# Optimization experiments

Hardware: AMD Instinct MI355X
Metric: run time of the kernel (lower is better)

Reference implementation:

```python
import jax, jax.numpy as jnp
import numpy as np
from jax import lax

B, T, D_IN, D_OUT = 8, 4096, 256, 256


def setup_inputs() -> dict:
    key = jax.random.key(0)
    k1, k2, k3, k4, k5 = jax.random.split(key, 5)
    bound_in = 1.0 / np.sqrt(D_IN)
    return {
        "inputs": jax.random.normal(k1, (B, T, D_IN), dtype=jnp.float32),
        "mask": jnp.zeros((B, T, 1), dtype=jnp.float32),
        "W_in": jax.random.uniform(k2, (D_OUT, D_IN), jnp.float32, -bound_in, bound_in),
        "b_in": jax.random.uniform(k3, (D_OUT,), jnp.float32, -bound_in, bound_in),
        "W_f": jax.random.uniform(k4, (D_OUT, D_IN), jnp.float32, -bound_in, bound_in),
        "b_f": jax.random.uniform(k5, (D_OUT,), jnp.float32, -bound_in, bound_in),
    }


def _forget_mult(f, x):
    # h_t = f_t * x_t + (1 - f_t) * h_{t-1}, h_{-1} = 0 (torchqrnn ForgetMult, hidden_init=None)
    fT = jnp.swapaxes(f, 0, 1)  # (T, B, D)
    xT = jnp.swapaxes(x, 0, 1)

    def step(h, fx):
        ft, xt = fx
        h = ft * xt + (1.0 - ft) * h
        return h, h

    h0 = jnp.zeros(xT.shape[1:], dtype=x.dtype)  # (B, D)
    _, hs = lax.scan(step, h0, (fT, xT))
    return jnp.swapaxes(hs, 0, 1)  # (B, T, D)


def reference(inputs, mask, W_in, b_in, W_f, b_f):
    # right_to_left = False -> no flips
    x = jnp.tanh(jnp.einsum("btd,od->bto", inputs, W_in) + b_in)
    f = jax.nn.sigmoid(jnp.einsum("btd,od->bto", inputs, W_f) + b_f + mask * 10000.0)
    return _forget_mult(f, x)
```

## Files before the change

kernel.cpp:

```cpp
#include <hip/hip_runtime.h>
#include <math.h>


typedef _Float16 f16x8 __attribute__((ext_vector_type(8)));
typedef float f32x4 __attribute__((ext_vector_type(4)));
typedef float f32x16 __attribute__((ext_vector_type(16)));
typedef unsigned int u32x4 __attribute__((ext_vector_type(4)));

constexpr int B_ = 8, T_ = 4096, D_ = 256, K_ = 256;
constexpr int M_ = B_ * T_;
constexpr int CHUNK = 64;
constexpr int NCH = T_ / CHUNK;
constexpr int NBLK = M_ / CHUNK;
constexpr int SLICE_EL = 8192;

struct alignas(4) XF { _Float16 x, f; };
struct alignas(4) HP2 { _Float16 h, p; };
union UHP { unsigned int u; HP2 hp; XF xf; };

__device__ __forceinline__ float fexp2(float a) { return __builtin_amdgcn_exp2f(a); }
__device__ __forceinline__ float frcp(float a) { return __builtin_amdgcn_rcpf(a); }
constexpr float L2E = 1.4426950408889634f;

__device__ __forceinline__ float fast_sigmoid(float z) {
  return frcp(1.f + fexp2(-z * L2E));
}
__device__ __forceinline__ float fast_tanh(float z) {
  const float t = fexp2(-2.f * L2E * fabsf(z));
  return copysignf((1.f - t) * frcp(1.f + t), z);
}

__global__ __launch_bounds__(256) void wconv(const float* __restrict__ Win,
                                             const float* __restrict__ Wf,
                                             _Float16* __restrict__ Wh2) {
  const int t = blockIdx.x * 256 + threadIdx.x;
  const int n = t & 255;
  const int kc = (t >> 8) & 1;
  const int mat = (t >> 9) & 1;
  const int kk2 = t >> 10;
  const float* s = (mat ? Wf : Win) + (size_t)n * K_ + kk2 * 16 + kc * 8;
  f32x4 a = *(const f32x4*)s;
  f32x4 b = *(const f32x4*)(s + 4);
  f16x8 o;
  o[0] = (_Float16)a[0]; o[1] = (_Float16)a[1];
  o[2] = (_Float16)a[2]; o[3] = (_Float16)a[3];
  o[4] = (_Float16)b[0]; o[5] = (_Float16)b[1];
  o[6] = (_Float16)b[2]; o[7] = (_Float16)b[3];
  *(f16x8*)(Wh2 + (size_t)t * 8) = o;
}

__global__ __launch_bounds__(256, 3) void gemm_hp(
    const float* __restrict__ A, const _Float16* __restrict__ Wh2,
    const float* __restrict__ bin, const float* __restrict__ bfv,
    const float* __restrict__ mask, unsigned int* __restrict__ HPout,
    float* __restrict__ Ap, float* __restrict__ Hp) {
  __shared__ __align__(16) char smem[49152];
  char* ldsA = smem;
  char* ldsW = smem + 32768;

  const int tid = threadIdx.x;
  const int w = tid >> 6, lane = tid & 63;
  const int mw = w >> 1, nw = w & 1;
  const int nl = lane & 31, kh = lane >> 5;
  const int ml = mw * 32 + nl;
  const int g = blockIdx.x;
  const int row0 = g * CHUNK;

  f32x16 acc[2][4];
#pragma unroll
  for (int mat = 0; mat < 2; ++mat)
#pragma unroll
    for (int nt = 0; nt < 4; ++nt) acc[mat][nt] = (f32x16)(0.f);

  {
    const int am = tid >> 2;
    const int ak4 = (tid & 3) * 8;
    const float* agp = A + (size_t)(row0 + am) * K_ + ak4 * 8;
#pragma unroll
    for (int j = 0; j < 8; ++j) {
      const int kcg = ak4 + j;
      f32x4 lo = *(const f32x4*)(agp + j * 8);
      f32x4 hi = *(const f32x4*)(agp + j * 8 + 4);
      f16x8 t;
      t[0] = (_Float16)lo[0]; t[1] = (_Float16)lo[1];
      t[2] = (_Float16)lo[2]; t[3] = (_Float16)lo[3];
      t[4] = (_Float16)hi[0]; t[5] = (_Float16)hi[1];
      t[6] = (_Float16)hi[2]; t[7] = (_Float16)hi[3];
      *(f16x8*)(ldsA + am * 512 + ((kcg ^ (am & 31)) << 4)) = t;
    }
  }
  __syncthreads();

  f16x8 wreg[4];
#pragma unroll
  for (int j = 0; j < 4; ++j)
    wreg[j] = *(const f16x8*)(Wh2 + (size_t)(j * 256 + tid) * 8);

  for (int kk2 = 0; kk2 < 16; ++kk2) {
#pragma unroll
    for (int j = 0; j < 4; ++j)
      *(f16x8*)(ldsW + (size_t)(j * 256 + tid) * 16) = wreg[j];
    if (kk2 < 15) {
#pragma unroll
      for (int j = 0; j < 4; ++j)
        wreg[j] = *(const f16x8*)(Wh2 + (size_t)(kk2 + 1) * SLICE_EL +
                                  (size_t)(j * 256 + tid) * 8);
    }
    __syncthreads();
    f16x8 afr;
    {
      const int kcg = kk2 * 2 + kh;
      afr = *(const f16x8*)(ldsA + ml * 512 + ((kcg ^ (ml & 31)) << 4));
    }
#pragma unroll
    for (int mat = 0; mat < 2; ++mat)
#pragma unroll
      for (int nt = 0; nt < 4; ++nt) {
        const int n = nw * 128 + nt * 32 + nl;
        f16x8 bfr = *(const f16x8*)(ldsW + (size_t)((mat * 2 + kh) * 256 + n) * 16);
        acc[mat][nt] = __builtin_amdgcn_mfma_f32_32x32x16_f16(
            afr, bfr, acc[mat][nt], 0, 0, 0);
      }
    __syncthreads();
  }

  float bx[4], bf[4];
#pragma unroll
  for (int nt = 0; nt < 4; ++nt) {
    const int col = nw * 128 + nt * 32 + nl;
    bx[nt] = bin[col];
    bf[nt] = bfv[col];
  }
  float madd[16];
#pragma unroll
  for (int reg = 0; reg < 16; ++reg) {
    const int rl = mw * 32 + (reg & 3) + 8 * (reg >> 2) + 4 * kh;
    madd[reg] = 10000.f * mask[row0 + rl];
  }

  const int d = tid;
  float hrun = 0.f, Prun = 1.f;
#pragma unroll
  for (int p = 0; p < 2; ++p) {
    if (mw == p) {
#pragma unroll
      for (int nt = 0; nt < 4; ++nt) {
        const int col = nw * 128 + nt * 32 + nl;
#pragma unroll
        for (int reg = 0; reg < 16; ++reg) {
          const int rloc = (reg & 3) + 8 * (reg >> 2) + 4 * kh;
          const float zx = acc[0][nt][reg] + bx[nt];
          const float zf = acc[1][nt][reg] + bf[nt] + madd[reg];
          XF v;
          v.x = (_Float16)fast_tanh(zx);
          v.f = (_Float16)fast_sigmoid(zf);
          *(XF*)(smem + ((size_t)rloc * D_ + col) * 4) = v;
        }
      }
    }
    __syncthreads();
#pragma unroll 8
    for (int t = 0; t < 32; ++t) {
      char* slot = smem + ((size_t)t * D_ + d) * 4;
      const XF v = *(const XF*)slot;
      const float f = (float)v.f;
      const float a = 1.f - f;
      hrun = f * (float)v.x + a * hrun;
      Prun *= a;
      HP2 o;
      o.h = (_Float16)hrun;
      o.p = (_Float16)Prun;
      *(HP2*)slot = o;
    }
    __syncthreads();
#pragma unroll
    for (int j = 0; j < 8; ++j) {
      const int c = j * 256 + tid;
      u32x4 vv = *(const u32x4*)(smem + (size_t)c * 16);
      *(u32x4*)(HPout + (size_t)g * 16384 + (size_t)p * 8192 + (size_t)c * 4) = vv;
    }
    __syncthreads();
  }

  Ap[(size_t)g * D_ + d] = Prun;
  Hp[(size_t)g * D_ + d] = hrun;
}

__global__ __launch_bounds__(256) void scan_mid(const float* __restrict__ Ap,
                                                const float* __restrict__ Hp,
                                                float* __restrict__ hs) {
  const int b = blockIdx.x, d = threadIdx.x;
  float h = 0.f;
#pragma unroll 8
  for (int c = 0; c < NCH; ++c) {
    const size_t i = ((size_t)(b * NCH + c)) * D_ + d;
    hs[i] = h;
    h = Hp[i] + Ap[i] * h;
  }
}

__global__ __launch_bounds__(256) void final_k(const unsigned int* __restrict__ HP,
                                               const float* __restrict__ hs,
                                               float* __restrict__ out) {
  const int g = blockIdx.x;
  const int lane = threadIdx.x & 63, wv = threadIdx.x >> 6;
  const int d0 = lane * 4;
  const f32x4 h0 = *(const f32x4*)(hs + (size_t)g * D_ + d0);
#pragma unroll 4
  for (int tt = 0; tt < 16; ++tt) {
    const int t = wv * 16 + tt;
    const size_t idx = ((size_t)g * CHUNK + t) * D_ + d0;
    u32x4 u = *(const u32x4*)(HP + idx);
    f32x4 o;
#pragma unroll
    for (int i = 0; i < 4; ++i) {
      UHP q; q.u = u[i];
      o[i] = (float)q.hp.h + (float)q.hp.p * h0[i];
    }
    *(f32x4*)(out + idx) = o;
  }
}

extern "C" void kernel_launch(void* const* d_in, const int* in_sizes, int n_in,
                              void* d_out, int out_size, void* d_ws, size_t ws_size,
                              hipStream_t stream) {
  const float* inputs = (const float*)d_in[0];
  const float* mask   = (const float*)d_in[1];
  const float* W_in   = (const float*)d_in[2];
  const float* b_in   = (const float*)d_in[3];
  const float* W_f    = (const float*)d_in[4];
  const float* b_f    = (const float*)d_in[5];
  float* out = (float*)d_out;
  char* ws = (char*)d_ws;

  constexpr size_t HPSZ = (size_t)M_ * D_ * 4;
  constexpr size_t WSZ  = (size_t)2 * 256 * 256 * 2;
  constexpr size_t SUM  = (size_t)NBLK * D_ * sizeof(float);

  unsigned int* HPb = (unsigned int*)ws;
  _Float16* Wh2 = (_Float16*)(ws + HPSZ);
  float* Ap = (float*)(ws + HPSZ + WSZ);
  float* Hp = (float*)(ws + HPSZ + WSZ + SUM);
  float* hs = (float*)(ws + HPSZ + WSZ + 2 * SUM);

  wconv<<<64, 256, 0, stream>>>(W_in, W_f, Wh2);
  gemm_hp<<<NBLK, 256, 0, stream>>>(inputs, Wh2, b_in, b_f, mask, HPb, Ap, Hp);
  scan_mid<<<B_, 256, 0, stream>>>(Ap, Hp, hs);
  final_k<<<NBLK, 256, 0, stream>>>(HPb, hs, out);
}
```

Measured before the change: 128.0 us.

## Fold cross-chunk scan into final kernel and retile GEMM waves over columns

```diff
diff --git a/kernel.cpp b/kernel.cpp
--- a/kernel.cpp
+++ b/kernel.cpp
@@ -60,17 +60,17 @@
 
   const int tid = threadIdx.x;
   const int w = tid >> 6, lane = tid & 63;
-  const int mw = w >> 1, nw = w & 1;
   const int nl = lane & 31, kh = lane >> 5;
-  const int ml = mw * 32 + nl;
   const int g = blockIdx.x;
   const int row0 = g * CHUNK;
 
-  f32x16 acc[2][4];
+  f32x16 acc[2][2][2];
 #pragma unroll
   for (int mat = 0; mat < 2; ++mat)
 #pragma unroll
-    for (int nt = 0; nt < 4; ++nt) acc[mat][nt] = (f32x16)(0.f);
+    for (int mt = 0; mt < 2; ++mt)
+#pragma unroll
+      for (int nt = 0; nt < 2; ++nt) acc[mat][mt][nt] = (f32x16)(0.f);
 
   {
     const int am = tid >> 2;
@@ -107,55 +107,59 @@
                                   (size_t)(j * 256 + tid) * 8);
     }
     __syncthreads();
-    f16x8 afr;
-    {
+    f16x8 afr[2];
+#pragma unroll
+    for (int mt = 0; mt < 2; ++mt) {
+      const int ml = mt * 32 + nl;
       const int kcg = kk2 * 2 + kh;
-      afr = *(const f16x8*)(ldsA + ml * 512 + ((kcg ^ (ml & 31)) << 4));
+      afr[mt] = *(const f16x8*)(ldsA + ml * 512 + ((kcg ^ (ml & 31)) << 4));
     }
 #pragma unroll
     for (int mat = 0; mat < 2; ++mat)
 #pragma unroll
-      for (int nt = 0; nt < 4; ++nt) {
-        const int n = nw * 128 + nt * 32 + nl;
+      for (int nt = 0; nt < 2; ++nt) {
+        const int n = w * 64 + nt * 32 + nl;
         f16x8 bfr = *(const f16x8*)(ldsW + (size_t)((mat * 2 + kh) * 256 + n) * 16);
-        acc[mat][nt] = __builtin_amdgcn_mfma_f32_32x32x16_f16(
-            afr, bfr, acc[mat][nt], 0, 0, 0);
+#pragma unroll
+        for (int mt = 0; mt < 2; ++mt)
+          acc[mat][mt][nt] = __builtin_amdgcn_mfma_f32_32x32x16_f16(
+              afr[mt], bfr, acc[mat][mt][nt], 0, 0, 0);
       }
     __syncthreads();
   }
 
-  float bx[4], bf[4];
-#pragma unroll
-  for (int nt = 0; nt < 4; ++nt) {
-    const int col = nw * 128 + nt * 32 + nl;
+  float bx[2], bf[2];
+#pragma unroll
+  for (int nt = 0; nt < 2; ++nt) {
+    const int col = w * 64 + nt * 32 + nl;
     bx[nt] = bin[col];
     bf[nt] = bfv[col];
   }
-  float madd[16];
-#pragma unroll
-  for (int reg = 0; reg < 16; ++reg) {
-    const int rl = mw * 32 + (reg & 3) + 8 * (reg >> 2) + 4 * kh;
-    madd[reg] = 10000.f * mask[row0 + rl];
-  }
+  float madd[2][16];
+#pragma unroll
+  for (int mt = 0; mt < 2; ++mt)
+#pragma unroll
+    for (int reg = 0; reg < 16; ++reg) {
+      const int rl = mt * 32 + (reg & 3) + 8 * (reg >> 2) + 4 * kh;
+      madd[mt][reg] = 10000.f * mask[row0 + rl];
+    }
 
   const int d = tid;
   float hrun = 0.f, Prun = 1.f;
 #pragma unroll
   for (int p = 0; p < 2; ++p) {
-    if (mw == p) {
-#pragma unroll
-      for (int nt = 0; nt < 4; ++nt) {
-        const int col = nw * 128 + nt * 32 + nl;
-#pragma unroll
-        for (int reg = 0; reg < 16; ++reg) {
-          const int rloc = (reg & 3) + 8 * (reg >> 2) + 4 * kh;
-          const float zx = acc[0][nt][reg] + bx[nt];
-          const float zf = acc[1][nt][reg] + bf[nt] + madd[reg];
-          XF v;
-          v.x = (_Float16)fast_tanh(zx);
-          v.f = (_Float16)fast_sigmoid(zf);
-          *(XF*)(smem + ((size_t)rloc * D_ + col) * 4) = v;
-        }
+#pragma unroll
+    for (int nt = 0; nt < 2; ++nt) {
+      const int col = w * 64 + nt * 32 + nl;
+#pragma unroll
+      for (int reg = 0; reg < 16; ++reg) {
+        const int rloc = (reg & 3) + 8 * (reg >> 2) + 4 * kh;
+        const float zx = acc[0][p][nt][reg] + bx[nt];
+        const float zf = acc[1][p][nt][reg] + bf[nt] + madd[p][reg];
+        XF v;
+        v.x = (_Float16)fast_tanh(zx);
+        v.f = (_Float16)fast_sigmoid(zf);
+        *(XF*)(smem + ((size_t)rloc * D_ + col) * 4) = v;
       }
     }
     __syncthreads();
@@ -186,26 +190,25 @@
   Hp[(size_t)g * D_ + d] = hrun;
 }
 
-__global__ __launch_bounds__(256) void scan_mid(const float* __restrict__ Ap,
-                                                const float* __restrict__ Hp,
-                                                float* __restrict__ hs) {
-  const int b = blockIdx.x, d = threadIdx.x;
-  float h = 0.f;
-#pragma unroll 8
-  for (int c = 0; c < NCH; ++c) {
-    const size_t i = ((size_t)(b * NCH + c)) * D_ + d;
-    hs[i] = h;
-    h = Hp[i] + Ap[i] * h;
-  }
-}
-
 __global__ __launch_bounds__(256) void final_k(const unsigned int* __restrict__ HP,
-                                               const float* __restrict__ hs,
+                                               const float* __restrict__ Ap,
+                                               const float* __restrict__ Hp,
                                                float* __restrict__ out) {
   const int g = blockIdx.x;
+  const int b = g >> 6, c = g & 63;
   const int lane = threadIdx.x & 63, wv = threadIdx.x >> 6;
   const int d0 = lane * 4;
-  const f32x4 h0 = *(const f32x4*)(hs + (size_t)g * D_ + d0);
+
+  f32x4 h0 = (f32x4){0.f, 0.f, 0.f, 0.f};
+  const size_t s0 = ((size_t)(b * NCH)) * D_ + d0;
+#pragma unroll 4
+  for (int j = 0; j < c; ++j) {
+    const f32x4 ap = *(const f32x4*)(Ap + s0 + (size_t)j * D_);
+    const f32x4 hp = *(const f32x4*)(Hp + s0 + (size_t)j * D_);
+#pragma unroll
+    for (int i = 0; i < 4; ++i) h0[i] = hp[i] + ap[i] * h0[i];
+  }
+
 #pragma unroll 4
   for (int tt = 0; tt < 16; ++tt) {
     const int t = wv * 16 + tt;
@@ -241,10 +244,8 @@
   _Float16* Wh2 = (_Float16*)(ws + HPSZ);
   float* Ap = (float*)(ws + HPSZ + WSZ);
   float* Hp = (float*)(ws + HPSZ + WSZ + SUM);
-  float* hs = (float*)(ws + HPSZ + WSZ + 2 * SUM);
 
   wconv<<<64, 256, 0, stream>>>(W_in, W_f, Wh2);
   gemm_hp<<<NBLK, 256, 0, stream>>>(inputs, Wh2, b_in, b_f, mask, HPb, Ap, Hp);
-  scan_mid<<<B_, 256, 0, stream>>>(Ap, Hp, hs);
-  final_k<<<NBLK, 256, 0, stream>>>(HPb, hs, out);
-}
+  final_k<<<NBLK, 256, 0, stream>>>(HPb, Ap, Hp, out);
+}
```

New measurement: 188.9 us. 47.5% more time.
